# Kernel optimization log

Measured on AMD Instinct MI355X. Metric: run time of the kernel, lower is better.

## Reference

```python
import jax, jax.numpy as jnp
import numpy as np

B, T, C, H = 8, 2048, 768, 64  # batch, seq_len, embedding_dim, head_size


def setup_inputs() -> dict:
    key = jax.random.key(0)
    k1, k2, k3, k4 = jax.random.split(key, 4)
    x = jax.random.normal(k1, (B, T, C), dtype=jnp.float32)
    attention_mask = jnp.ones((B, T), dtype=jnp.float32)
    # nn.Linear(C, H, bias=False) weights stored pre-transposed as (C, H)
    scale = 0.02
    Wq = jax.random.normal(k2, (C, H), dtype=jnp.float32) * scale
    Wk = jax.random.normal(k3, (C, H), dtype=jnp.float32) * scale
    Wv = jax.random.normal(k4, (C, H), dtype=jnp.float32) * scale
    return {"x": x, "attention_mask": attention_mask, "Wq": Wq, "Wk": Wk, "Wv": Wv}


def reference(x, attention_mask, Wq, Wk, Wv):
    # x: [B,T,C]; attention_mask: [B,T] (multiplied per query row)
    head_size = Wq.shape[-1]
    q = x @ Wq  # [B,T,H]
    k = x @ Wk  # [B,T,H]
    v = x @ Wv  # [B,T,H]
    inv_sqrt_h = jnp.asarray(1.0 / np.sqrt(head_size), x.dtype)
    s = jnp.einsum('bqh,bkh->bqk', q, k) * inv_sqrt_h  # [B,T,T]
    # attention_mask.unsqueeze(2) * qK ; masked_fill(qK == 0, -inf)
    s = attention_mask[:, :, None] * s
    s = jnp.where(s == 0, -jnp.inf, s)
    # causal tril mask
    seq = x.shape[1]
    tril = jnp.tril(jnp.ones((seq, seq), dtype=bool))
    s = jnp.where(tril[None, :, :], s, -jnp.inf)
    p = jax.nn.softmax(s, axis=-1)
    # dropout p=0.0 -> identity; nan cleanup (fully-masked rows)
    p = jnp.where(jnp.isnan(p), jnp.asarray(0.0, p.dtype), p)
    out = jnp.einsum('bqk,bkh->bqh', p, v)  # [B,T,H]
    return out
```

## Files before the change

### kernel.cpp

```cpp
#include <hip/hip_runtime.h>
#include <hip/hip_bf16.h>

#define B_ 8
#define T_ 2048
#define C_ 768
#define H_ 64
#define BT_ (B_*T_)

typedef __attribute__((ext_vector_type(8))) short bf16x8;
typedef __attribute__((ext_vector_type(4))) float f32x4;

__device__ __forceinline__ unsigned short f2bf(float x) {
    __hip_bfloat16 h = __float2bfloat16(x);
    return __builtin_bit_cast(unsigned short, h);
}

__device__ __forceinline__ bf16x8 cvt8(float4 a, float4 b) {
    bf16x8 r;
    r[0] = (short)f2bf(a.x); r[1] = (short)f2bf(a.y);
    r[2] = (short)f2bf(a.z); r[3] = (short)f2bf(a.w);
    r[4] = (short)f2bf(b.x); r[5] = (short)f2bf(b.y);
    r[6] = (short)f2bf(b.z); r[7] = (short)f2bf(b.w);
    return r;
}

__global__ __launch_bounds__(256) void wprep(
    const float* __restrict__ Wq, const float* __restrict__ Wk,
    const float* __restrict__ Wv, unsigned short* __restrict__ WTf)
{
    __shared__ float tile[32][68];
    const int bid = blockIdx.x;
    const int m = bid / 24, gc = bid % 24;
    const float* __restrict__ W = (m == 0) ? Wq : (m == 1) ? Wk : Wv;
    const int t = threadIdx.x;
    {
        const int r = t >> 3, c0 = (t & 7) * 8;
        float4 a = *(const float4*)(W + (size_t)(gc * 32 + r) * H_ + c0);
        float4 b = *(const float4*)(W + (size_t)(gc * 32 + r) * H_ + c0 + 4);
        *(float4*)&tile[r][c0]     = a;
        *(float4*)&tile[r][c0 + 4] = b;
    }
    __syncthreads();
    const int fl = t >> 6, lane = t & 63;
    const int q16 = lane & 15, quad = lane >> 4;
    const int f = m * 4 + fl;
    ushort4 u0, u1;
    u0.x = f2bf(tile[quad * 8 + 0][fl * 16 + q16]);
    u0.y = f2bf(tile[quad * 8 + 1][fl * 16 + q16]);
    u0.z = f2bf(tile[quad * 8 + 2][fl * 16 + q16]);
    u0.w = f2bf(tile[quad * 8 + 3][fl * 16 + q16]);
    u1.x = f2bf(tile[quad * 8 + 4][fl * 16 + q16]);
    u1.y = f2bf(tile[quad * 8 + 5][fl * 16 + q16]);
    u1.z = f2bf(tile[quad * 8 + 6][fl * 16 + q16]);
    u1.w = f2bf(tile[quad * 8 + 7][fl * 16 + q16]);
    unsigned short* __restrict__ dst = WTf + ((size_t)(gc * 12 + f) * 64 + lane) * 8;
    *(ushort4*)(dst)     = u0;
    *(ushort4*)(dst + 4) = u1;
}

__global__ __launch_bounds__(256, 2) void qkv_kernel(
    const float* __restrict__ x, const unsigned short* __restrict__ WTf,
    unsigned short* __restrict__ qF, unsigned short* __restrict__ kF,
    unsigned short* __restrict__ vF)
{
    __shared__ float mrg[3][64][49];
    const int tid  = threadIdx.x;
    const int w    = tid >> 6;
    const int lane = tid & 63;
    const int q16  = lane & 15, quad = lane >> 4;
    const int rowBase = blockIdx.x << 5;

    const float* __restrict__ xp0 = x + (size_t)(rowBase + q16) * C_ + w * 192 + quad * 8;
    const float* __restrict__ xp1 = xp0 + (size_t)16 * C_;

    f32x4 acc0[12] = {}, acc1[12] = {};
    #pragma unroll
    for (int c = 0; c < 6; c++) {
        const int gc = w * 6 + c;
        const unsigned short* __restrict__ wpc = WTf + ((size_t)gc * 12) * 512 + lane * 8;
        float4 xa0 = *(const float4*)(xp0 + c * 32);
        float4 xb0 = *(const float4*)(xp0 + c * 32 + 4);
        float4 xa1 = *(const float4*)(xp1 + c * 32);
        float4 xb1 = *(const float4*)(xp1 + c * 32 + 4);
        bf16x8 wf[12];
        #pragma unroll
        for (int f = 0; f < 12; f++)
            wf[f] = *(const bf16x8*)(wpc + f * 512);
        bf16x8 xf0 = cvt8(xa0, xb0);
        bf16x8 xf1 = cvt8(xa1, xb1);
        #pragma unroll
        for (int f = 0; f < 12; f++) {
            acc0[f] = __builtin_amdgcn_mfma_f32_16x16x32_bf16(wf[f], xf0, acc0[f], 0, 0, 0);
            acc1[f] = __builtin_amdgcn_mfma_f32_16x16x32_bf16(wf[f], xf1, acc1[f], 0, 0, 0);
        }
    }

    auto flush = [&](f32x4* acc, int gtile) {
        const size_t gt = (size_t)gtile;
        #pragma unroll
        for (int f = 0; f < 8; f++) {
            ushort4 u;
            u.x = f2bf(acc[f][0]); u.y = f2bf(acc[f][1]);
            u.z = f2bf(acc[f][2]); u.w = f2bf(acc[f][3]);
            const int n4 = f & 3;
            const int qp = (2 * n4 + (quad >> 1)) & 3;
            const int j0 = (quad & 1) * 4;
            unsigned short* __restrict__ dst = (f < 4) ? qF : kF;
            *(ushort4*)(dst + ((gt * 2 + (n4 >> 1)) * 64 + q16 + 16 * qp) * 8 + j0) = u;
        }
        const size_t g32 = (size_t)(gtile >> 1);
        const int qv = (gtile & 1) * 2 + (q16 >> 3);
        const int jv = q16 & 7;
        #pragma unroll
        for (int f = 8; f < 12; f++)
            #pragma unroll
            for (int r = 0; r < 4; r++)
                vF[((g32 * 4 + (f - 8)) * 64 + quad * 4 + r + 16 * qv) * 8 + jv] =
                    f2bf(acc[f][r]);
    };

    if (w > 0) {
        #pragma unroll
        for (int f = 0; f < 12; f++)
            #pragma unroll
            for (int r = 0; r < 4; r++) mrg[w - 1][lane][f * 4 + r] = acc0[f][r];
    }
    __syncthreads();
    if (w == 0) {
        #pragma unroll
        for (int j = 0; j < 3; j++)
            #pragma unroll
            for (int f = 0; f < 12; f++)
                #pragma unroll
                for (int r = 0; r < 4; r++) acc0[f][r] += mrg[j][lane][f * 4 + r];
        flush(acc0, rowBase >> 4);
    }
    __syncthreads();
    if (w > 0) {
        #pragma unroll
        for (int f = 0; f < 12; f++)
            #pragma unroll
            for (int r = 0; r < 4; r++) mrg[w - 1][lane][f * 4 + r] = acc1[f][r];
    }
    __syncthreads();
    if (w == 0) {
        #pragma unroll
        for (int j = 0; j < 3; j++)
            #pragma unroll
            for (int f = 0; f < 12; f++)
                #pragma unroll
                for (int r = 0; r < 4; r++) acc1[f][r] += mrg[j][lane][f * 4 + r];
        flush(acc1, (rowBase >> 4) + 1);
    }
}

__global__ __launch_bounds__(256) void attn_kernel(
    const unsigned short* __restrict__ qF, const unsigned short* __restrict__ kF,
    const unsigned short* __restrict__ vF, const float* __restrict__ mask,
    float* __restrict__ out)
{
    __shared__ __align__(16) unsigned short pS[4][16][88];
    __shared__ float oS[3][64][17];
    __shared__ float mlS[3][64][2];

    const int tid  = threadIdx.x;
    const int w    = tid >> 6;
    const int lane = tid & 63;
    const int q16  = lane & 15;
    const int quad = lane >> 4;
    const int bid  = blockIdx.x;
    const int b    = bid & 7;
    const int qt   = 127 - (bid >> 3);
    const int qrow = (qt << 4) + q16;

    const size_t qbase = ((size_t)(b * 128 + qt) * 2) * 512 + lane * 8;
    bf16x8 qf0 = *(const bf16x8*)(qF + qbase);
    bf16x8 qf1 = *(const bf16x8*)(qF + qbase + 512);
    const float maskv = mask[b * T_ + qrow] * 0.125f * 1.44269504f;

    f32x4 o[4] = {};
    float m_run = -__builtin_inff();
    float l_run = 0.f;

    const int niter = ((qt << 4) + 16 + 63) >> 6;
    for (int kt = w; kt < niter; kt += 4) {
        const int kbase = kt << 6;

        bf16x8 kf[8], vf[8];
        #pragma unroll
        for (int sub = 0; sub < 4; sub++) {
            const unsigned short* kp = kF + ((size_t)(b * 128 + kt * 4 + sub) * 2) * 512 + lane * 8;
            kf[2 * sub]     = *(const bf16x8*)(kp);
            kf[2 * sub + 1] = *(const bf16x8*)(kp + 512);
        }
        #pragma unroll
        for (int ht = 0; ht < 4; ht++) {
            const unsigned short* vp = vF + ((size_t)(b * 64 + kt * 2) * 4 + ht) * 512 + lane * 8;
            vf[2 * ht]     = *(const bf16x8*)(vp);
            vf[2 * ht + 1] = *(const bf16x8*)(vp + 4 * 512);
        }

        f32x4 sa[4] = {};
        #pragma unroll
        for (int sub = 0; sub < 4; sub++) {
            sa[sub] = __builtin_amdgcn_mfma_f32_16x16x32_bf16(kf[2 * sub],     qf0, sa[sub], 0, 0, 0);
            sa[sub] = __builtin_amdgcn_mfma_f32_16x16x32_bf16(kf[2 * sub + 1], qf1, sa[sub], 0, 0, 0);
        }

        float s[16];
        #pragma unroll
        for (int sub = 0; sub < 4; sub++)
            #pragma unroll
            for (int r = 0; r < 4; r++) {
                int kidx = kbase + sub * 16 + quad * 4 + r;
                float sv = sa[sub][r] * maskv;
                sv = (sv == 0.f) ? -__builtin_inff() : sv;
                sv = (kidx > qrow) ? -__builtin_inff() : sv;
                s[sub * 4 + r] = sv;
            }

        float mx = s[0];
        #pragma unroll
        for (int i2 = 1; i2 < 16; i2++) mx = fmaxf(mx, s[i2]);
        mx = fmaxf(mx, __shfl_xor(mx, 16));
        mx = fmaxf(mx, __shfl_xor(mx, 32));
        float m_new = fmaxf(m_run, mx);
        float m_use = (m_new == -__builtin_inff()) ? 0.f : m_new;
        float alpha = exp2f(m_run - m_use);
        float p[16], psum = 0.f;
        #pragma unroll
        for (int i2 = 0; i2 < 16; i2++) { p[i2] = exp2f(s[i2] - m_use); psum += p[i2]; }
        psum += __shfl_xor(psum, 16);
        psum += __shfl_xor(psum, 32);
        l_run = l_run * alpha + psum;
        m_run = m_new;
        #pragma unroll
        for (int ht = 0; ht < 4; ht++)
            #pragma unroll
            for (int r = 0; r < 4; r++) o[ht][r] *= alpha;

        #pragma unroll
        for (int sub = 0; sub < 4; sub++) {
            unsigned int lo = (unsigned int)f2bf(p[sub * 4 + 0]) | ((unsigned int)f2bf(p[sub * 4 + 1]) << 16);
            unsigned int hi = (unsigned int)f2bf(p[sub * 4 + 2]) | ((unsigned int)f2bf(p[sub * 4 + 3]) << 16);
            *(uint2*)&pS[w][q16][sub * 16 + quad * 4] = make_uint2(lo, hi);
        }
        bf16x8 pf0 = *(const bf16x8*)&pS[w][q16][quad * 8];
        bf16x8 pf1 = *(const bf16x8*)&pS[w][q16][32 + quad * 8];

        #pragma unroll
        for (int ht = 0; ht < 4; ht++) {
            o[ht] = __builtin_amdgcn_mfma_f32_16x16x32_bf16(vf[2 * ht],     pf0, o[ht], 0, 0, 0);
            o[ht] = __builtin_amdgcn_mfma_f32_16x16x32_bf16(vf[2 * ht + 1], pf1, o[ht], 0, 0, 0);
        }
    }

    if (w > 0) {
        mlS[w - 1][lane][0] = m_run;
        mlS[w - 1][lane][1] = l_run;
        #pragma unroll
        for (int ht = 0; ht < 4; ht++)
            #pragma unroll
            for (int r = 0; r < 4; r++) oS[w - 1][lane][ht * 4 + r] = o[ht][r];
    }
    __syncthreads();
    if (w == 0) {
        float mm[3], ll[3];
        float m = m_run;
        #pragma unroll
        for (int j = 0; j < 3; j++) {
            mm[j] = mlS[j][lane][0]; ll[j] = mlS[j][lane][1];
            m = fmaxf(m, mm[j]);
        }
        float mu = (m == -__builtin_inff()) ? 0.f : m;
        float a0 = exp2f(m_run - mu);
        float aj[3];
        float l = l_run * a0;
        #pragma unroll
        for (int j = 0; j < 3; j++) { aj[j] = exp2f(mm[j] - mu); l += ll[j] * aj[j]; }
        float invl = (l > 0.f) ? (1.f / l) : 0.f;
        #pragma unroll
        for (int ht = 0; ht < 4; ht++) {
            float4 ov;
            float vx = o[ht][0] * a0, vy = o[ht][1] * a0, vz = o[ht][2] * a0, vw2 = o[ht][3] * a0;
            #pragma unroll
            for (int j = 0; j < 3; j++) {
                vx += oS[j][lane][ht * 4 + 0] * aj[j];
                vy += oS[j][lane][ht * 4 + 1] * aj[j];
                vz += oS[j][lane][ht * 4 + 2] * aj[j];
                vw2 += oS[j][lane][ht * 4 + 3] * aj[j];
            }
            ov.x = vx * invl; ov.y = vy * invl; ov.z = vz * invl; ov.w = vw2 * invl;
            *(float4*)(out + ((size_t)(b * T_) + qrow) * H_ + ht * 16 + quad * 4) = ov;
        }
    }
}

extern "C" void kernel_launch(void* const* d_in, const int* in_sizes, int n_in,
                              void* d_out, int out_size, void* d_ws, size_t ws_size,
                              hipStream_t stream) {
    const float* x    = (const float*)d_in[0];
    const float* mask = (const float*)d_in[1];
    const float* Wq   = (const float*)d_in[2];
    const float* Wk   = (const float*)d_in[3];
    const float* Wv   = (const float*)d_in[4];
    float* out = (float*)d_out;

    unsigned short* qf = (unsigned short*)d_ws;
    unsigned short* kf = qf + (size_t)BT_ * H_;
    unsigned short* vf = kf + (size_t)BT_ * H_;
    unsigned short* wt = vf + (size_t)BT_ * H_;

    wprep<<<72, 256, 0, stream>>>(Wq, Wk, Wv, wt);
    qkv_kernel<<<BT_ / 32, 256, 0, stream>>>(x, wt, qf, kf, vf);
    attn_kernel<<<B_ * (T_ / 16), 256, 0, stream>>>(qf, kf, vf, mask, out);
}
```

Before: 120.3 us.

## Shrink QKV projection tile to 16 rows with coalesced bf16 x staging in LDS

The QKV projection block now covers 16 rows instead of 32 and launches twice as many blocks, with launch bounds raised to 4 blocks per CU. The x rows are loaded coalesced, converted to bf16 once, and staged in shared memory that aliases the reduction buffer. This is meant to raise occupancy and improve global load coalescing for the memory-bound x read. In exchange each weight fragment is reused across only one row tile, which doubles total weight traffic from L2, and an extra barrier is added.

```diff
diff --git a/kernel.cpp b/kernel.cpp
--- a/kernel.cpp
+++ b/kernel.cpp
@@ -58,45 +58,67 @@
     *(ushort4*)(dst + 4) = u1;
 }
 
-__global__ __launch_bounds__(256, 2) void qkv_kernel(
+__global__ __launch_bounds__(256, 4) void qkv_kernel(
     const float* __restrict__ x, const unsigned short* __restrict__ WTf,
     unsigned short* __restrict__ qF, unsigned short* __restrict__ kF,
     unsigned short* __restrict__ vF)
 {
-    __shared__ float mrg[3][64][49];
+    __shared__ __align__(16) char shraw[3 * 64 * 49 * 4];
+    unsigned short* xS = (unsigned short*)shraw;
+    float (*mrg)[64][49] = (float (*)[64][49])shraw;
+
     const int tid  = threadIdx.x;
     const int w    = tid >> 6;
     const int lane = tid & 63;
     const int q16  = lane & 15, quad = lane >> 4;
-    const int rowBase = blockIdx.x << 5;
-
-    const float* __restrict__ xp0 = x + (size_t)(rowBase + q16) * C_ + w * 192 + quad * 8;
-    const float* __restrict__ xp1 = xp0 + (size_t)16 * C_;
-
-    f32x4 acc0[12] = {}, acc1[12] = {};
+    const int rowBase = blockIdx.x << 4;
+
+    {
+        const int r = tid >> 4, l = tid & 15;
+        const float* __restrict__ xrow = x + (size_t)(rowBase + r) * C_;
+        #pragma unroll
+        for (int i = 0; i < 6; i++) {
+            const int j = i * 16 + l;
+            float4 a = *(const float4*)(xrow + j * 8);
+            float4 b = *(const float4*)(xrow + j * 8 + 4);
+            *(bf16x8*)&xS[(size_t)r * 772 + j * 8] = cvt8(a, b);
+        }
+    }
+    __syncthreads();
+
+    const unsigned short* __restrict__ xrowS = xS + q16 * 772 + w * 192 + quad * 8;
+    f32x4 acc[12] = {};
     #pragma unroll
     for (int c = 0; c < 6; c++) {
         const int gc = w * 6 + c;
         const unsigned short* __restrict__ wpc = WTf + ((size_t)gc * 12) * 512 + lane * 8;
-        float4 xa0 = *(const float4*)(xp0 + c * 32);
-        float4 xb0 = *(const float4*)(xp0 + c * 32 + 4);
-        float4 xa1 = *(const float4*)(xp1 + c * 32);
-        float4 xb1 = *(const float4*)(xp1 + c * 32 + 4);
+        bf16x8 xf = *(const bf16x8*)(xrowS + c * 32);
         bf16x8 wf[12];
         #pragma unroll
         for (int f = 0; f < 12; f++)
             wf[f] = *(const bf16x8*)(wpc + f * 512);
-        bf16x8 xf0 = cvt8(xa0, xb0);
-        bf16x8 xf1 = cvt8(xa1, xb1);
-        #pragma unroll
-        for (int f = 0; f < 12; f++) {
-            acc0[f] = __builtin_amdgcn_mfma_f32_16x16x32_bf16(wf[f], xf0, acc0[f], 0, 0, 0);
-            acc1[f] = __builtin_amdgcn_mfma_f32_16x16x32_bf16(wf[f], xf1, acc1[f], 0, 0, 0);
-        }
-    }
-
-    auto flush = [&](f32x4* acc, int gtile) {
-        const size_t gt = (size_t)gtile;
+        #pragma unroll
+        for (int f = 0; f < 12; f++)
+            acc[f] = __builtin_amdgcn_mfma_f32_16x16x32_bf16(wf[f], xf, acc[f], 0, 0, 0);
+    }
+    __syncthreads();
+
+    if (w > 0) {
+        #pragma unroll
+        for (int f = 0; f < 12; f++)
+            #pragma unroll
+            for (int r = 0; r < 4; r++) mrg[w - 1][lane][f * 4 + r] = acc[f][r];
+    }
+    __syncthreads();
+    if (w == 0) {
+        #pragma unroll
+        for (int j = 0; j < 3; j++)
+            #pragma unroll
+            for (int f = 0; f < 12; f++)
+                #pragma unroll
+                for (int r = 0; r < 4; r++) acc[f][r] += mrg[j][lane][f * 4 + r];
+
+        const size_t gt = (size_t)(rowBase >> 4);
         #pragma unroll
         for (int f = 0; f < 8; f++) {
             ushort4 u;
@@ -108,8 +130,8 @@
             unsigned short* __restrict__ dst = (f < 4) ? qF : kF;
             *(ushort4*)(dst + ((gt * 2 + (n4 >> 1)) * 64 + q16 + 16 * qp) * 8 + j0) = u;
         }
-        const size_t g32 = (size_t)(gtile >> 1);
-        const int qv = (gtile & 1) * 2 + (q16 >> 3);
+        const size_t g32 = gt >> 1;
+        const int qv = ((int)gt & 1) * 2 + (q16 >> 3);
         const int jv = q16 & 7;
         #pragma unroll
         for (int f = 8; f < 12; f++)
@@ -117,40 +139,6 @@
             for (int r = 0; r < 4; r++)
                 vF[((g32 * 4 + (f - 8)) * 64 + quad * 4 + r + 16 * qv) * 8 + jv] =
                     f2bf(acc[f][r]);
-    };
-
-    if (w > 0) {
-        #pragma unroll
-        for (int f = 0; f < 12; f++)
-            #pragma unroll
-            for (int r = 0; r < 4; r++) mrg[w - 1][lane][f * 4 + r] = acc0[f][r];
-    }
-    __syncthreads();
-    if (w == 0) {
-        #pragma unroll
-        for (int j = 0; j < 3; j++)
-            #pragma unroll
-            for (int f = 0; f < 12; f++)
-                #pragma unroll
-                for (int r = 0; r < 4; r++) acc0[f][r] += mrg[j][lane][f * 4 + r];
-        flush(acc0, rowBase >> 4);
-    }
-    __syncthreads();
-    if (w > 0) {
-        #pragma unroll
-        for (int f = 0; f < 12; f++)
-            #pragma unroll
-            for (int r = 0; r < 4; r++) mrg[w - 1][lane][f * 4 + r] = acc1[f][r];
-    }
-    __syncthreads();
-    if (w == 0) {
-        #pragma unroll
-        for (int j = 0; j < 3; j++)
-            #pragma unroll
-            for (int f = 0; f < 12; f++)
-                #pragma unroll
-                for (int r = 0; r < 4; r++) acc1[f][r] += mrg[j][lane][f * 4 + r];
-        flush(acc1, (rowBase >> 4) + 1);
     }
 }
 
@@ -312,6 +300,6 @@
     unsigned short* wt = vf + (size_t)BT_ * H_;
 
     wprep<<<72, 256, 0, stream>>>(Wq, Wk, Wv, wt);
-    qkv_kernel<<<BT_ / 32, 256, 0, stream>>>(x, wt, qf, kf, vf);
+    qkv_kernel<<<BT_ / 16, 256, 0, stream>>>(x, wt, qf, kf, vf);
     attn_kernel<<<B_ * (T_ / 16), 256, 0, stream>>>(qf, kf, vf, mask, out);
 }
```

Result: no change. 118.1 us (-1.8%).
